# Optimization experiments

Hardware: AMD Instinct MI355X
Metric: run time of the kernel (lower is better)

Reference implementation:

```python
import jax, jax.numpy as jnp
import numpy as np

B, N, C = 128, 8732, 21  # batch, SSD priors, VOC classes (incl. background)
EPS = 1e-7


def setup_inputs() -> dict:
    key = jax.random.key(0)
    k1, k2, k3 = jax.random.split(key, 3)
    return {
        "lam": jnp.float32(0.7),
        "conf": jax.random.uniform(k1, (B, N, C), dtype=jnp.float32),
        "conf_shuffle": jax.random.uniform(k2, (B, N, C), dtype=jnp.float32),
        "conf_interpolation": jax.random.uniform(k3, (B, N, C), dtype=jnp.float32),
    }


def reference(lam, conf, conf_shuffle, conf_interpolation):
    half = conf.shape[0] // 2
    # swap the two halves of the shuffled batch
    conf_temp = jnp.concatenate([conf_shuffle[half:], conf_shuffle[:half]], axis=0)

    # foreground mask: max class score beats background score, on both sides
    left_mask = jnp.max(conf[..., 1:], axis=-1) > conf[..., 0]
    right_mask = jnp.max(conf_temp[..., 1:], axis=-1) > conf_temp[..., 0]
    mask = (left_mask & right_mask).astype(conf.dtype)  # [B, N]

    mixed = lam * conf + (1.0 - lam) * conf_temp + EPS
    inter = conf_interpolation + EPS

    sg = jax.lax.stop_gradient
    # KLDivLoss(log_input, target) = target * (log(target) - log_input), summed over classes
    inter_t = sg(inter)
    kl_a = jnp.sum(inter_t * (jnp.log(inter_t) - jnp.log(mixed)), axis=-1)  # [B, N]
    mixed_t = sg(mixed)
    kl_b = jnp.sum(mixed_t * (jnp.log(mixed_t) - jnp.log(inter)), axis=-1)  # [B, N]

    cnt = jnp.sum(mask)
    # masked mean over selected (b, n) samples; 0 if mask empty
    loss = jnp.sum((kl_a + kl_b) * mask) / jnp.maximum(cnt, 1.0)
    return jnp.where(cnt > 0, loss / 2.0, jnp.float32(0.0))
```

## Files before the change

### kernel.cpp

```cpp
#include <hip/hip_runtime.h>


#define EPS 1e-7f

constexpr int B = 128;
constexpr int N = 8732;
constexpr int C = 21;
constexpr int ROWS = B * N;
constexpr int ELEMS = ROWS * C;
constexpr int HALF_ELEMS = (B / 2) * N * C;
constexpr int RPI = 3;
constexpr int GELEMS = RPI * C;
constexpr int NGROUPS = (ROWS + RPI - 1) / RPI;
constexpr int BLOCK = 256;
constexpr int GRID = 2048;
constexpr int NWAVES = GRID * (BLOCK / 64);

__global__ __launch_bounds__(BLOCK, 6) void isd_main_kernel(
    const float* __restrict__ lam_p,
    const float* __restrict__ conf,
    const float* __restrict__ csh,
    const float* __restrict__ cin,
    double* __restrict__ partials)
{
    const int tid  = threadIdx.x;
    const int lane = tid & 63;
    const int wid  = (blockIdx.x * BLOCK + tid) >> 6;

    const int dr    = lane / 21;
    const int cpos  = lane - dr * 21;
    const int gbase = dr * 21;
    const unsigned long long gm = 0x1FFFFFull;

    const float lam = lam_p[0];
    const float oml = 1.0f - lam;

    double bs = 0.0, bc = 0.0;

    for (int g = wid; g < NGROUPS; g += NWAVES) {
        const int e     = g * GELEMS + lane;
        const bool valid = (lane < GELEMS) && (e < ELEMS);
        const int ec    = valid ? e : (ELEMS - 1);

        const float cv  = conf[ec];
        const float ivr = cin[ec];
        const int e2    = ec + ((ec < HALF_ELEMS) ? HALF_ELEMS : -HALF_ELEMS);
        const float tv  = csh[e2];

        const float iv = ivr + EPS;
        const float mv = fmaf(lam, cv, oml * tv) + EPS;
        float klt = (iv - mv) * (__logf(iv) - __logf(mv));
        klt = valid ? klt : 0.0f;

        const float c0 = __shfl(cv, gbase, 64);
        const float t0 = __shfl(tv, gbase, 64);
        const unsigned long long balc = __ballot(cv > c0);
        const unsigned long long balt = __ballot(tv > t0);

        #pragma unroll
        for (int off = 16; off > 0; off >>= 1) {
            const float o = __shfl(klt, lane + off, 64);
            if (cpos + off < 21) klt += o;
        }

        if (cpos == 0 && valid) {
            const bool fg = (((balc >> lane) & gm) != 0ull) &&
                            (((balt >> lane) & gm) != 0ull);
            if (fg) { bs += (double)klt; bc += 1.0; }
        }
    }

    #pragma unroll
    for (int off = 32; off > 0; off >>= 1) {
        bs += __shfl_down(bs, off, 64);
        bc += __shfl_down(bc, off, 64);
    }

    __shared__ double r_sum[BLOCK / 64];
    __shared__ double r_cnt[BLOCK / 64];
    const int wave = tid >> 6;
    if ((tid & 63) == 0) { r_sum[wave] = bs; r_cnt[wave] = bc; }
    __syncthreads();

    if (tid == 0) {
        double s = 0.0, c = 0.0;
        #pragma unroll
        for (int w = 0; w < BLOCK / 64; ++w) { s += r_sum[w]; c += r_cnt[w]; }
        partials[2 * blockIdx.x + 0] = s;
        partials[2 * blockIdx.x + 1] = c;
    }
}

__global__ __launch_bounds__(256) void isd_final_kernel(
    const double* __restrict__ partials,
    float* __restrict__ out)
{
    double s = 0.0, c = 0.0;
    for (int i = threadIdx.x; i < GRID; i += 256) {
        s += partials[2 * i + 0];
        c += partials[2 * i + 1];
    }
    #pragma unroll
    for (int off = 32; off > 0; off >>= 1) {
        s += __shfl_down(s, off, 64);
        c += __shfl_down(c, off, 64);
    }
    __shared__ double ss[4], sc[4];
    const int wave = threadIdx.x >> 6;
    const int lane = threadIdx.x & 63;
    if (lane == 0) { ss[wave] = s; sc[wave] = c; }
    __syncthreads();
    if (threadIdx.x == 0) {
        const double S  = ss[0] + ss[1] + ss[2] + ss[3];
        const double Cc = sc[0] + sc[1] + sc[2] + sc[3];
        out[0] = (Cc > 0.0) ? (float)(S / fmax(Cc, 1.0) * 0.5) : 0.0f;
    }
}

extern "C" void kernel_launch(void* const* d_in, const int* in_sizes, int n_in,
                              void* d_out, int out_size, void* d_ws, size_t ws_size,
                              hipStream_t stream) {
    const float* lam  = (const float*)d_in[0];
    const float* conf = (const float*)d_in[1];
    const float* csh  = (const float*)d_in[2];
    const float* cin  = (const float*)d_in[3];
    float* out = (float*)d_out;
    double* partials = (double*)d_ws;

    isd_main_kernel<<<GRID, BLOCK, 0, stream>>>(lam, conf, csh, cin, partials);
    isd_final_kernel<<<1, 256, 0, stream>>>(partials, out);
}
```

Before: 269.1 us.

## Unroll grid-stride loop 4x and defer per-row KL reduction to the end

Each wave now handles four groups per loop trip, so more global loads are in flight at once. The per-iteration segmented shuffle reduction across the 21 class lanes is removed. Instead, each lane accumulates its own masked KL term and the wave reduces once at the end. The foreground count becomes a float per lane, and the launch-bounds occupancy hint drops from 6 to 4, which gives each thread more registers at the cost of resident waves.

```diff
diff --git a/kernel.cpp b/kernel.cpp
--- a/kernel.cpp
+++ b/kernel.cpp
@@ -9,14 +9,13 @@
 constexpr int ROWS = B * N;
 constexpr int ELEMS = ROWS * C;
 constexpr int HALF_ELEMS = (B / 2) * N * C;
-constexpr int RPI = 3;
-constexpr int GELEMS = RPI * C;
-constexpr int NGROUPS = (ROWS + RPI - 1) / RPI;
+constexpr int GELEMS = 63;
+constexpr int NGROUPS = (ROWS + 2) / 3;
 constexpr int BLOCK = 256;
 constexpr int GRID = 2048;
 constexpr int NWAVES = GRID * (BLOCK / 64);
 
-__global__ __launch_bounds__(BLOCK, 6) void isd_main_kernel(
+__global__ __launch_bounds__(BLOCK, 4) void isd_main_kernel(
     const float* __restrict__ lam_p,
     const float* __restrict__ conf,
     const float* __restrict__ csh,
@@ -25,61 +24,64 @@
 {
     const int tid  = threadIdx.x;
     const int lane = tid & 63;
-    const int wid  = (blockIdx.x * BLOCK + tid) >> 6;
+    const int wid  = __builtin_amdgcn_readfirstlane(
+                         blockIdx.x * (BLOCK / 64) + (tid >> 6));
 
-    const int dr    = lane / 21;
-    const int cpos  = lane - dr * 21;
-    const int gbase = dr * 21;
-    const unsigned long long gm = 0x1FFFFFull;
+    const int dr   = lane / 21;
+    const int cpos = lane - dr * 21;
+    const int gb   = dr * 21;
+    const bool lane_ok = lane < GELEMS;
 
     const float lam = lam_p[0];
     const float oml = 1.0f - lam;
 
-    double bs = 0.0, bc = 0.0;
+    double bs = 0.0;
+    float  bc = 0.0f;
 
-    for (int g = wid; g < NGROUPS; g += NWAVES) {
-        const int e     = g * GELEMS + lane;
-        const bool valid = (lane < GELEMS) && (e < ELEMS);
-        const int ec    = valid ? e : (ELEMS - 1);
+    auto body = [&](int g) {
+        const int  e     = g * GELEMS + lane;
+        const bool valid = lane_ok && (e < ELEMS);
+        const int  ec    = valid ? e : 0;
 
         const float cv  = conf[ec];
         const float ivr = cin[ec];
-        const int e2    = ec + ((ec < HALF_ELEMS) ? HALF_ELEMS : -HALF_ELEMS);
+        const int   e2  = ec + ((ec < HALF_ELEMS) ? HALF_ELEMS : -HALF_ELEMS);
         const float tv  = csh[e2];
 
         const float iv = ivr + EPS;
         const float mv = fmaf(lam, cv, oml * tv) + EPS;
-        float klt = (iv - mv) * (__logf(iv) - __logf(mv));
-        klt = valid ? klt : 0.0f;
+        const float klt = (iv - mv) * (__logf(iv) - __logf(mv));
 
-        const float c0 = __shfl(cv, gbase, 64);
-        const float t0 = __shfl(tv, gbase, 64);
+        const float c0 = __shfl(cv, gb, 64);
+        const float t0 = __shfl(tv, gb, 64);
         const unsigned long long balc = __ballot(cv > c0);
         const unsigned long long balt = __ballot(tv > t0);
+        const bool fg = (((balc >> gb) & 0x1FFFFFull) != 0ull) &&
+                        (((balt >> gb) & 0x1FFFFFull) != 0ull);
 
-        #pragma unroll
-        for (int off = 16; off > 0; off >>= 1) {
-            const float o = __shfl(klt, lane + off, 64);
-            if (cpos + off < 21) klt += o;
-        }
+        const float m = (fg && valid) ? 1.0f : 0.0f;
+        bs += (double)(klt * m);
+        bc += (cpos == 0) ? m : 0.0f;
+    };
 
-        if (cpos == 0 && valid) {
-            const bool fg = (((balc >> lane) & gm) != 0ull) &&
-                            (((balt >> lane) & gm) != 0ull);
-            if (fg) { bs += (double)klt; bc += 1.0; }
-        }
+    for (int g = wid; g < NGROUPS; g += 4 * NWAVES) {
+        body(g);
+        body(g + 1 * NWAVES);
+        body(g + 2 * NWAVES);
+        body(g + 3 * NWAVES);
     }
 
+    double bcD = (double)bc;
     #pragma unroll
     for (int off = 32; off > 0; off >>= 1) {
-        bs += __shfl_down(bs, off, 64);
-        bc += __shfl_down(bc, off, 64);
+        bs  += __shfl_down(bs,  off, 64);
+        bcD += __shfl_down(bcD, off, 64);
     }
 
     __shared__ double r_sum[BLOCK / 64];
     __shared__ double r_cnt[BLOCK / 64];
     const int wave = tid >> 6;
-    if ((tid & 63) == 0) { r_sum[wave] = bs; r_cnt[wave] = bc; }
+    if ((tid & 63) == 0) { r_sum[wave] = bs; r_cnt[wave] = bcD; }
     __syncthreads();
 
     if (tid == 0) {
```

New measurement: 278.6 us. 1.04x slower.
